# Kernel optimization log

Measured on AMD Instinct MI355X. Metric: run time of the kernel, lower is better.

The kernel has to match this reference:

```python
import jax, jax.numpy as jnp
import numpy as np

BN_EPS = 1e-5

def binary_activation(x):
    # ReActNet BinaryActivation: forward = sign(x), backward = piecewise poly STE
    out_fwd = jnp.sign(x)
    m1 = (x < -1.0).astype(x.dtype)
    m2 = (x < 0.0).astype(x.dtype)
    m3 = (x < 1.0).astype(x.dtype)
    out1 = -1.0 * m1 + (x * x + 2.0 * x) * (1.0 - m1)
    out2 = out1 * m2 + (-x * x + 2.0 * x) * (1.0 - m2)
    out3 = out2 * m3 + 1.0 * (1.0 - m3)
    return jax.lax.stop_gradient(out_fwd - out3) + out3

def binary_conv3x3(x, w, stride=1):
    # per-output-channel scaling = mean |w| over (in, kh, kw), detached
    scale = jax.lax.stop_gradient(jnp.mean(jnp.abs(w), axis=(1, 2, 3), keepdims=True))
    bw_no_grad = jax.lax.stop_gradient(scale * jnp.sign(w))
    cw = jnp.clip(w, -1.0, 1.0)
    bw = bw_no_grad - jax.lax.stop_gradient(cw) + cw
    return jax.lax.conv_general_dilated(
        x, bw, window_strides=(stride, stride), padding=[(1, 1), (1, 1)],
        dimension_numbers=('NCHW', 'OIHW', 'NCHW'))

def batchnorm_inference(y, gamma, beta, mean, var):
    inv = gamma * jax.lax.rsqrt(var + BN_EPS)
    return y * inv[None, :, None, None] + (beta - mean * inv)[None, :, None, None]

def setup_inputs() -> dict:
    key = jax.random.key(0)
    k1, k2, k3 = jax.random.split(key, 3)
    N, Cin, Cout, H, W = 64, 128, 128, 56, 56
    x = jax.random.normal(k1, (N, Cin, H, W), dtype=jnp.float32)
    weight = jax.random.normal(k2, (Cout, Cin, 3, 3), dtype=jnp.float32) * 0.1
    gamma = jnp.ones((Cout,), dtype=jnp.float32)
    beta = jnp.zeros((Cout,), dtype=jnp.float32)
    bn_mean = jnp.zeros((Cout,), dtype=jnp.float32)
    bn_var = jax.random.uniform(k3, (Cout,), dtype=jnp.float32)
    return {"x": x, "weight": weight, "gamma": gamma, "beta": beta,
            "bn_mean": bn_mean, "bn_var": bn_var}

def reference(x, weight, gamma, beta, bn_mean, bn_var):
    residual = x
    out = binary_activation(x)
    out = binary_conv3x3(out, weight, stride=1)
    out = batchnorm_inference(out, gamma, beta, bn_mean, bn_var)
    return out + residual
```

## Files before the change

kernel.cpp:

```cpp
#include <hip/hip_runtime.h>


#define N_   64
#define C_   128
#define H_   56
#define W_   56
#define HW_  (H_*W_)
#define PH_  (H_+2)
#define PW_  (W_+2)
#define PHW_ (PH_*PW_)
#define NPIX (N_*HW_)
#define NPAD (N_*PHW_)

typedef unsigned long long u64;

__global__ void prep_w_kernel(const float* __restrict__ w,
                              const float* __restrict__ gamma,
                              const float* __restrict__ beta,
                              const float* __restrict__ bn_mean,
                              const float* __restrict__ bn_var,
                              u64* __restrict__ wbits,
                              float* __restrict__ A, float* __restrict__ B) {
    const int o = blockIdx.x;
    const int lane = threadIdx.x;
    const float* wo = w + o * 1152;

    float s = 0.f;
    #pragma unroll
    for (int k = 0; k < 18; k++) s += fabsf(wo[k * 64 + lane]);
    #pragma unroll
    for (int off = 32; off > 0; off >>= 1) s += __shfl_down(s, off);
    float scale = __shfl(s, 0) * (1.0f / 1152.0f);

    #pragma unroll
    for (int t = 0; t < 9; t++) {
        #pragma unroll
        for (int j = 0; j < 2; j++) {
            float v = wo[(j * 64 + lane) * 9 + t];
            u64 b = __ballot(v < 0.0f);
            if (lane == 0) wbits[(o * 9 + t) * 2 + j] = b;
        }
    }
    if (lane == 0) {
        float inv = gamma[o] * rsqrtf(bn_var[o] + 1e-5f);
        A[o] = scale * inv;
        B[o] = beta[o] - bn_mean[o] * inv;
    }
}

__global__ __launch_bounds__(256) void pack_x_kernel(
        const float* __restrict__ x,
        ulonglong2* __restrict__ xbs,
        ulonglong2* __restrict__ xbz,
        unsigned* __restrict__ xcnt) {
    int g = blockIdx.x * 256 + threadIdx.x;
    int n  = g / PHW_;
    int r  = g - n * PHW_;
    int ph = r / PW_;
    int pw = r - ph * PW_;
    int h = ph - 1, w = pw - 1;

    unsigned p[4] = {0,0,0,0};
    unsigned z[4] = {0,0,0,0};

    if ((unsigned)h < (unsigned)H_ && (unsigned)w < (unsigned)W_) {
        const unsigned* xp =
            (const unsigned*)(x + (size_t)n * C_ * HW_ + h * W_ + w);
        #pragma unroll
        for (int j = 0; j < 4; j++) {
            unsigned pj = 0, zj = 0;
            #pragma unroll
            for (int c = 0; c < 32; c++) {
                unsigned u = xp[(size_t)(j * 32 + c) * HW_];
                pj |= (u >> 31) << c;
                zj |= ((u << 1) != 0u ? 1u : 0u) << c;
            }
            p[j] = pj; z[j] = zj;
        }
    }
    ulonglong2 s2, z2;
    s2.x = (u64)p[0] | ((u64)p[1] << 32);
    s2.y = (u64)p[2] | ((u64)p[3] << 32);
    z2.x = (u64)z[0] | ((u64)z[1] << 32);
    z2.y = (u64)z[2] | ((u64)z[3] << 32);
    xbs[g] = s2;
    xbz[g] = z2;
    xcnt[g] = __popc(z[0]) + __popc(z[1]) + __popc(z[2]) + __popc(z[3]);
}

__device__ __forceinline__ int tapmask_of(int idx) {
    int tm = 0;
    if (idx & 1) tm |= 0x007;
    if (idx & 2) tm |= 0x1C0;
    if (idx & 4) tm |= 0x049;
    if (idx & 8) tm |= 0x124;
    return tm;
}

__global__ __launch_bounds__(256, 6) void bconv_kernel(
        const ulonglong2* __restrict__ xbs,
        const ulonglong2* __restrict__ xbz,
        const unsigned*   __restrict__ xcnt,
        const ulonglong2* __restrict__ wbits,
        const float* __restrict__ Ag, const float* __restrict__ Bg,
        const float* __restrict__ x, float* __restrict__ out) {
    __shared__ ulonglong2 w_s[576];
    __shared__ int   psum_s[16 * 64];
    __shared__ float A_s[64], B_s[64];

    const int tid = threadIdx.x;
    const int obase = blockIdx.y * 64;

    for (int i = tid; i < 576; i += 256) w_s[i] = wbits[obase * 9 + i];
    if (tid < 64) { A_s[tid] = Ag[obase + tid]; B_s[tid] = Bg[obase + tid]; }
    __syncthreads();

    for (int e = tid; e < 1024; e += 256) {
        int idx = e >> 6, o = e & 63;
        int tm = tapmask_of(idx);
        int s = 0;
        #pragma unroll
        for (int t = 0; t < 9; t++) {
            if ((tm >> t) & 1) {
                ulonglong2 ww = w_s[o * 9 + t];
                s += 128 - 2 * (__popcll(ww.x) + __popcll(ww.y));
            }
        }
        psum_s[e] = s;
    }
    __syncthreads();

    int g = blockIdx.x * 256 + tid;
    int n = g / HW_;
    int r = g - n * HW_;
    int h = r / W_;
    int w = r - h * W_;
    int pb = (n * PH_ + h + 1) * PW_ + (w + 1);

    u64 sx[9], sy[9];
    int taps_off[9];
    int csum = 0;
    #pragma unroll
    for (int dh = 0; dh < 3; dh++) {
        #pragma unroll
        for (int dw = 0; dw < 3; dw++) {
            int k = dh * 3 + dw;
            int idx = pb + (dh - 1) * PW_ + (dw - 1);
            taps_off[k] = idx;
            ulonglong2 t2 = xbs[idx];
            sx[k] = t2.x; sy[k] = t2.y;
            csum += (int)xcnt[idx];
        }
    }

    int pidx = (h == 0 ? 1 : 0) | (h == H_-1 ? 2 : 0) |
               (w == 0 ? 4 : 0) | (w == W_-1 ? 8 : 0);
    int valid = 9 - __popc(tapmask_of(pidx));
    bool slow = (csum != 128 * valid);

    const float* xr = x   + ((size_t)n * C_ + obase) * HW_ + r;
    float*       op = out + ((size_t)n * C_ + obase) * HW_ + r;
    const int* psp = &psum_s[pidx * 64];

    if (!slow) {
        #pragma unroll 2
        for (int o = 0; o < 64; o++) {
            int pc = 0;
            #pragma unroll
            for (int k = 0; k < 9; k++) {
                ulonglong2 ww = w_s[o * 9 + k];
                pc += __popcll(sx[k] ^ ww.x);
                pc += __popcll(sy[k] ^ ww.y);
            }
            int dot = 1152 - 2 * pc - psp[o];
            op[o * HW_] = fmaf(A_s[o], (float)dot, B_s[o]) + xr[o * HW_];
        }
    } else {
        for (int o = 0; o < 64; o++) {
            int pc = 0;
            #pragma unroll
            for (int k = 0; k < 9; k++) {
                ulonglong2 ww = w_s[o * 9 + k];
                ulonglong2 zz = xbz[taps_off[k]];
                pc += __popcll((sx[k] ^ ww.x) & zz.x);
                pc += __popcll((sy[k] ^ ww.y) & zz.y);
            }
            int dot = csum - 2 * pc;
            op[o * HW_] = fmaf(A_s[o], (float)dot, B_s[o]) + xr[o * HW_];
        }
    }
}

extern "C" void kernel_launch(void* const* d_in, const int* in_sizes, int n_in,
                              void* d_out, int out_size, void* d_ws, size_t ws_size,
                              hipStream_t stream) {
    const float* x      = (const float*)d_in[0];
    const float* weight = (const float*)d_in[1];
    const float* gamma  = (const float*)d_in[2];
    const float* beta   = (const float*)d_in[3];
    const float* bnmean = (const float*)d_in[4];
    const float* bnvar  = (const float*)d_in[5];
    float* out = (float*)d_out;

    char* ws = (char*)d_ws;
    u64*        wbits = (u64*)ws;
    float*      A     = (float*)(ws + 18432);
    float*      B     = (float*)(ws + 18944);
    ulonglong2* xbs   = (ulonglong2*)(ws + 19456);
    ulonglong2* xbz   = (ulonglong2*)(ws + 19456 + (size_t)NPAD * 16);
    unsigned*   xcnt  = (unsigned*)(ws + 19456 + (size_t)NPAD * 32);

    prep_w_kernel<<<128, 64, 0, stream>>>(weight, gamma, beta, bnmean, bnvar,
                                          wbits, A, B);
    pack_x_kernel<<<NPAD / 256, 256, 0, stream>>>(x, xbs, xbz, xcnt);
    dim3 cgrid(NPIX / 256, 2);
    bconv_kernel<<<cgrid, 256, 0, stream>>>(xbs, xbz, xcnt,
                                            (const ulonglong2*)wbits, A, B,
                                            x, out);
}
```

Before: 280.8 us.

## Pack two pixels per thread with float2 loads, separate border zeroing, read weights via scalar loads

The pack kernel now handles two adjacent interior pixels per thread using float2 loads and writes them into the padded layout. A separate small kernel zeroes the padding border. The conv kernel drops its weight staging in LDS and reads packed weights straight from global memory at wave-uniform addresses, which should become scalar loads. It also folds the per-border popcount correction into a precomputed bias pair. The aim is better load vectorisation in packing, less LDS traffic and fewer syncs in the conv, at the cost of an extra launch and reliance on scalar/L1 caching for the weights.

```diff
diff --git a/kernel.cpp b/kernel.cpp
--- a/kernel.cpp
+++ b/kernel.cpp
@@ -53,39 +53,65 @@
         ulonglong2* __restrict__ xbs,
         ulonglong2* __restrict__ xbz,
         unsigned* __restrict__ xcnt) {
-    int g = blockIdx.x * 256 + threadIdx.x;
-    int n  = g / PHW_;
-    int r  = g - n * PHW_;
-    int ph = r / PW_;
-    int pw = r - ph * PW_;
-    int h = ph - 1, w = pw - 1;
-
-    unsigned p[4] = {0,0,0,0};
-    unsigned z[4] = {0,0,0,0};
-
-    if ((unsigned)h < (unsigned)H_ && (unsigned)w < (unsigned)W_) {
-        const unsigned* xp =
-            (const unsigned*)(x + (size_t)n * C_ * HW_ + h * W_ + w);
-        #pragma unroll
-        for (int j = 0; j < 4; j++) {
-            unsigned pj = 0, zj = 0;
-            #pragma unroll
-            for (int c = 0; c < 32; c++) {
-                unsigned u = xp[(size_t)(j * 32 + c) * HW_];
-                pj |= (u >> 31) << c;
-                zj |= ((u << 1) != 0u ? 1u : 0u) << c;
-            }
-            p[j] = pj; z[j] = zj;
-        }
-    }
+    int t = blockIdx.x * 256 + threadIdx.x;
+    int p = t * 2;
+    int n = p / HW_;
+    int r = p - n * HW_;
+    int h = r / W_;
+    int w = r - h * W_;
+
+    const float2* xp = (const float2*)(x + (size_t)n * C_ * HW_ + h * W_ + w);
+
+    unsigned pa[4], za[4], pb[4], zb[4];
+    #pragma unroll
+    for (int j = 0; j < 4; j++) { pa[j]=0; za[j]=0; pb[j]=0; zb[j]=0; }
+
+    #pragma unroll
+    for (int j = 0; j < 4; j++) {
+        unsigned paj = 0, zaj = 0, pbj = 0, zbj = 0;
+        #pragma unroll 16
+        for (int c = 0; c < 32; c++) {
+            float2 v = xp[(size_t)(j * 32 + c) * (HW_ / 2)];
+            unsigned ua = __float_as_uint(v.x);
+            unsigned ub = __float_as_uint(v.y);
+            paj |= (ua >> 31) << c;
+            zaj |= ((ua << 1) != 0u ? 1u : 0u) << c;
+            pbj |= (ub >> 31) << c;
+            zbj |= ((ub << 1) != 0u ? 1u : 0u) << c;
+        }
+        pa[j]=paj; za[j]=zaj; pb[j]=pbj; zb[j]=zbj;
+    }
+
+    int pg = (n * PH_ + h + 1) * PW_ + (w + 1);
     ulonglong2 s2, z2;
-    s2.x = (u64)p[0] | ((u64)p[1] << 32);
-    s2.y = (u64)p[2] | ((u64)p[3] << 32);
-    z2.x = (u64)z[0] | ((u64)z[1] << 32);
-    z2.y = (u64)z[2] | ((u64)z[3] << 32);
-    xbs[g] = s2;
-    xbz[g] = z2;
-    xcnt[g] = __popc(z[0]) + __popc(z[1]) + __popc(z[2]) + __popc(z[3]);
+    s2.x = (u64)pa[0] | ((u64)pa[1] << 32);
+    s2.y = (u64)pa[2] | ((u64)pa[3] << 32);
+    z2.x = (u64)za[0] | ((u64)za[1] << 32);
+    z2.y = (u64)za[2] | ((u64)za[3] << 32);
+    xbs[pg] = s2; xbz[pg] = z2;
+    xcnt[pg] = __popc(za[0]) + __popc(za[1]) + __popc(za[2]) + __popc(za[3]);
+
+    s2.x = (u64)pb[0] | ((u64)pb[1] << 32);
+    s2.y = (u64)pb[2] | ((u64)pb[3] << 32);
+    z2.x = (u64)zb[0] | ((u64)zb[1] << 32);
+    z2.y = (u64)zb[2] | ((u64)zb[3] << 32);
+    xbs[pg + 1] = s2; xbz[pg + 1] = z2;
+    xcnt[pg + 1] = __popc(zb[0]) + __popc(zb[1]) + __popc(zb[2]) + __popc(zb[3]);
+}
+
+__global__ void border_kernel(ulonglong2* __restrict__ xbs,
+                              ulonglong2* __restrict__ xbz,
+                              unsigned* __restrict__ xcnt) {
+    int bt = blockIdx.x * 256 + threadIdx.x;
+    if (bt >= N_ * 228) return;
+    int n = bt / 228, e = bt - n * 228;
+    int ph, pw;
+    if (e < 58)       { ph = 0;  pw = e; }
+    else if (e < 116) { ph = 57; pw = e - 58; }
+    else { int i = e - 116; ph = 1 + (i >> 1); pw = (i & 1) ? 57 : 0; }
+    int g = (n * PH_ + ph) * PW_ + pw;
+    ulonglong2 zz; zz.x = 0; zz.y = 0;
+    xbs[g] = zz; xbz[g] = zz; xcnt[g] = 0;
 }
 
 __device__ __forceinline__ int tapmask_of(int idx) {
@@ -101,32 +127,27 @@
         const ulonglong2* __restrict__ xbs,
         const ulonglong2* __restrict__ xbz,
         const unsigned*   __restrict__ xcnt,
-        const ulonglong2* __restrict__ wbits,
+        const u64* __restrict__ wbits,
         const float* __restrict__ Ag, const float* __restrict__ Bg,
         const float* __restrict__ x, float* __restrict__ out) {
-    __shared__ ulonglong2 w_s[576];
-    __shared__ int   psum_s[16 * 64];
-    __shared__ float A_s[64], B_s[64];
+    __shared__ float2 AB_s[16 * 64];
 
     const int tid = threadIdx.x;
     const int obase = blockIdx.y * 64;
 
-    for (int i = tid; i < 576; i += 256) w_s[i] = wbits[obase * 9 + i];
-    if (tid < 64) { A_s[tid] = Ag[obase + tid]; B_s[tid] = Bg[obase + tid]; }
-    __syncthreads();
-
     for (int e = tid; e < 1024; e += 256) {
-        int idx = e >> 6, o = e & 63;
+        int idx = e >> 6, o = (e & 63);
         int tm = tapmask_of(idx);
+        const u64* wp = wbits + (size_t)(obase + o) * 18;
         int s = 0;
         #pragma unroll
         for (int t = 0; t < 9; t++) {
-            if ((tm >> t) & 1) {
-                ulonglong2 ww = w_s[o * 9 + t];
-                s += 128 - 2 * (__popcll(ww.x) + __popcll(ww.y));
-            }
-        }
-        psum_s[e] = s;
+            if ((tm >> t) & 1)
+                s += 128 - 2 * (__popcll(wp[2*t]) + __popcll(wp[2*t+1]));
+        }
+        float a = Ag[obase + o];
+        float2 ab; ab.x = a; ab.y = Bg[obase + o] - a * (float)s;
+        AB_s[e] = ab;
     }
     __syncthreads();
 
@@ -160,33 +181,36 @@
 
     const float* xr = x   + ((size_t)n * C_ + obase) * HW_ + r;
     float*       op = out + ((size_t)n * C_ + obase) * HW_ + r;
-    const int* psp = &psum_s[pidx * 64];
+    const float2* abp = &AB_s[pidx << 6];
 
     if (!slow) {
+        const u64* wp = wbits + (size_t)obase * 18;
         #pragma unroll 2
         for (int o = 0; o < 64; o++) {
             int pc = 0;
             #pragma unroll
             for (int k = 0; k < 9; k++) {
-                ulonglong2 ww = w_s[o * 9 + k];
-                pc += __popcll(sx[k] ^ ww.x);
-                pc += __popcll(sy[k] ^ ww.y);
+                pc += __popcll(sx[k] ^ wp[2*k]);
+                pc += __popcll(sy[k] ^ wp[2*k+1]);
             }
-            int dot = 1152 - 2 * pc - psp[o];
-            op[o * HW_] = fmaf(A_s[o], (float)dot, B_s[o]) + xr[o * HW_];
+            wp += 18;
+            float2 ab = abp[o];
+            float dot = (float)(1152 - 2 * pc);
+            op[o * HW_] = fmaf(ab.x, dot, ab.y) + xr[o * HW_];
         }
     } else {
         for (int o = 0; o < 64; o++) {
+            const u64* wp = wbits + (size_t)(obase + o) * 18;
             int pc = 0;
             #pragma unroll
             for (int k = 0; k < 9; k++) {
-                ulonglong2 ww = w_s[o * 9 + k];
                 ulonglong2 zz = xbz[taps_off[k]];
-                pc += __popcll((sx[k] ^ ww.x) & zz.x);
-                pc += __popcll((sy[k] ^ ww.y) & zz.y);
+                pc += __popcll((sx[k] ^ wp[2*k])   & zz.x);
+                pc += __popcll((sy[k] ^ wp[2*k+1]) & zz.y);
             }
+            float a = abp[o].x;
             int dot = csum - 2 * pc;
-            op[o * HW_] = fmaf(A_s[o], (float)dot, B_s[o]) + xr[o * HW_];
+            op[o * HW_] = fmaf(a, (float)dot, Bg[obase + o]) + xr[o * HW_];
         }
     }
 }
@@ -212,9 +236,9 @@
 
     prep_w_kernel<<<128, 64, 0, stream>>>(weight, gamma, beta, bnmean, bnvar,
                                           wbits, A, B);
-    pack_x_kernel<<<NPAD / 256, 256, 0, stream>>>(x, xbs, xbz, xcnt);
+    pack_x_kernel<<<NPIX / 2 / 256, 256, 0, stream>>>(x, xbs, xbz, xcnt);
+    border_kernel<<<(N_ * 228 + 255) / 256, 256, 0, stream>>>(xbs, xbz, xcnt);
     dim3 cgrid(NPIX / 256, 2);
-    bconv_kernel<<<cgrid, 256, 0, stream>>>(xbs, xbz, xcnt,
-                                            (const ulonglong2*)wbits, A, B,
+    bconv_kernel<<<cgrid, 256, 0, stream>>>(xbs, xbz, xcnt, wbits, A, B,
                                             x, out);
 }
```

Measured after the change: 272.1 us. -3.1%, faster.
